# Optimization experiments

Measured on AMD Instinct MI355X. Metric: run time of the kernel, lower is better.

The kernel has to match this reference:

```python
import jax, jax.numpy as jnp
import numpy as np

SEQ, BATCH, N_IN, N_HID, N_OUT = 2048, 64, 256, 512, 128


def setup_inputs() -> dict:
    key = jax.random.key(0)
    ks = jax.random.split(key, 7)
    s_ih = 1.0 / np.sqrt(N_IN)
    s_hh = 1.0 / np.sqrt(N_HID)
    return {
        "x": jax.random.normal(ks[0], (SEQ, BATCH, N_IN), dtype=jnp.float32),
        # PyTorch Linear stores weight as (out_features, in_features)
        "W_ih": jax.random.uniform(ks[1], (N_HID, N_IN), jnp.float32, -s_ih, s_ih),
        "b_ih": jax.random.uniform(ks[2], (N_HID,), jnp.float32, -s_ih, s_ih),
        "W_hh": jax.random.uniform(ks[3], (N_HID, N_HID), jnp.float32, -s_hh, s_hh),
        "b_hh": jax.random.uniform(ks[4], (N_HID,), jnp.float32, -s_hh, s_hh),
        "W_ho": jax.random.uniform(ks[5], (N_OUT, N_HID), jnp.float32, -s_hh, s_hh),
        "b_ho": jax.random.uniform(ks[6], (N_OUT,), jnp.float32, -s_hh, s_hh),
    }


def reference(x, W_ih, b_ih, W_hh, b_hh, W_ho, b_ho):
    # hidden init: torch.zeros(1, n_hidden) broadcasts to (batch, n_hidden)
    h0 = jnp.zeros((x.shape[1], W_hh.shape[0]), dtype=x.dtype)

    def step(h, xt):
        # new_h = tanh(Linear_ih(x_t) + Linear_hh(h))
        h_new = jnp.tanh(xt @ W_ih.T + b_ih + h @ W_hh.T + b_hh)
        return h_new, None

    h_final, _ = jax.lax.scan(step, h0, x)
    return h_final @ W_ho.T + b_ho  # (batch, n_output)
```

## Files before the change

### kernel.cpp

```cpp
#include <hip/hip_runtime.h>
#include <math.h>

#define SEQ   2048
#define BATCH 64
#define NIN   256
#define NHID  512
#define NOUT  128

#define NSL 4
#define JSL 128

#define WIRE_WORDS (2*BATCH*NSL*256)
#define WIRE_BYTES ((size_t)WIRE_WORDS*4)
#define HFIN_BYTES ((size_t)BATCH*NHID*4)
#define XP_BYTES   ((size_t)SEQ*BATCH*NHID*4)

typedef unsigned int u32;
typedef u32 u32x2 __attribute__((ext_vector_type(2)));

__device__ __forceinline__ u32x2 ld8_ic(const u32* p) {
  u32x2 r;
  asm volatile("global_load_dwordx2 %0, %1, off sc0 sc1"
               : "=v"(r) : "v"(p) : "memory");
  return r;
}
__device__ __forceinline__ void st8_ic(u32* p, u32x2 v) {
  asm volatile("global_store_dwordx2 %0, %1, off sc0 sc1"
               :: "v"(p), "v"(v) : "memory");
}
__device__ __forceinline__ void wait_vm0() {
  asm volatile("s_waitcnt vmcnt(0)" ::: "memory");
  __builtin_amdgcn_sched_barrier(0);
}

__global__ __launch_bounds__(256, 1)
void xproj_kernel(const float* __restrict__ x,
                  const float* __restrict__ Wih,
                  const float* __restrict__ bih,
                  const float* __restrict__ bhh,
                  float* __restrict__ xp)
{
  const int bj = blockIdx.x & 7;
  const int bm = blockIdx.x >> 3;
  const int tid = threadIdx.x;
  const int tx = tid & 15, ty = tid >> 4;

  __shared__ __align__(16) float  wT[NIN][68];
  __shared__ __align__(16) float4 xS[64][66];

  for (int it = 0; it < 64; ++it) {
    const int widx = tid + (it << 8);
    const int k = widx >> 6, j = widx & 63;
    wT[k][j] = Wih[(size_t)(bj*64 + j)*NIN + k];
  }
  const int jg = bj*64 + tx*4;
  float4 bv;
  bv.x = bih[jg+0]+bhh[jg+0]; bv.y = bih[jg+1]+bhh[jg+1];
  bv.z = bih[jg+2]+bhh[jg+2]; bv.w = bih[jg+3]+bhh[jg+3];
  __syncthreads();

  for (int mt = 0; mt < 8; ++mt) {
    const size_t r0 = (size_t)bm*512 + mt*64;
    for (int it = 0; it < 16; ++it) {
      const int f = tid + (it << 8);
      const int m = f >> 6, kq = f & 63;
      xS[m][kq] = *(const float4*)&x[(r0 + m)*NIN + (kq << 2)];
    }
    __syncthreads();

    float acc[4][4];
    #pragma unroll
    for (int q = 0; q < 4; ++q)
      #pragma unroll
      for (int jj = 0; jj < 4; ++jj) acc[q][jj] = 0.f;

    for (int kq = 0; kq < 64; ++kq) {
      const float4 xv0 = xS[ty*4+0][kq];
      const float4 xv1 = xS[ty*4+1][kq];
      const float4 xv2 = xS[ty*4+2][kq];
      const float4 xv3 = xS[ty*4+3][kq];
      #pragma unroll
      for (int i = 0; i < 4; ++i) {
        const float4 wv = *(const float4*)&wT[(kq<<2)+i][tx*4];
        const float xi0 = (i==0)?xv0.x:(i==1)?xv0.y:(i==2)?xv0.z:xv0.w;
        const float xi1 = (i==0)?xv1.x:(i==1)?xv1.y:(i==2)?xv1.z:xv1.w;
        const float xi2 = (i==0)?xv2.x:(i==1)?xv2.y:(i==2)?xv2.z:xv2.w;
        const float xi3 = (i==0)?xv3.x:(i==1)?xv3.y:(i==2)?xv3.z:xv3.w;
        acc[0][0]=fmaf(xi0,wv.x,acc[0][0]); acc[0][1]=fmaf(xi0,wv.y,acc[0][1]);
        acc[0][2]=fmaf(xi0,wv.z,acc[0][2]); acc[0][3]=fmaf(xi0,wv.w,acc[0][3]);
        acc[1][0]=fmaf(xi1,wv.x,acc[1][0]); acc[1][1]=fmaf(xi1,wv.y,acc[1][1]);
        acc[1][2]=fmaf(xi1,wv.z,acc[1][2]); acc[1][3]=fmaf(xi1,wv.w,acc[1][3]);
        acc[2][0]=fmaf(xi2,wv.x,acc[2][0]); acc[2][1]=fmaf(xi2,wv.y,acc[2][1]);
        acc[2][2]=fmaf(xi2,wv.z,acc[2][2]); acc[2][3]=fmaf(xi2,wv.w,acc[2][3]);
        acc[3][0]=fmaf(xi3,wv.x,acc[3][0]); acc[3][1]=fmaf(xi3,wv.y,acc[3][1]);
        acc[3][2]=fmaf(xi3,wv.z,acc[3][2]); acc[3][3]=fmaf(xi3,wv.w,acc[3][3]);
      }
    }
    #pragma unroll
    for (int q = 0; q < 4; ++q) {
      float4 o;
      o.x = acc[q][0]+bv.x; o.y = acc[q][1]+bv.y;
      o.z = acc[q][2]+bv.z; o.w = acc[q][3]+bv.w;
      *(float4*)&xp[(r0 + ty*4 + q)*NHID + jg] = o;
    }
    __syncthreads();
  }
}

__global__ __launch_bounds__(512, 1)
void rnn_seq4_kernel(const float* __restrict__ xp,
                     const float* __restrict__ Whh,
                     u32* __restrict__ wire,
                     float* __restrict__ hfin)
{
  const int bid = blockIdx.x;
  const int sj  = bid >> 6;
  const int b   = bid & 63;
  const int tid = threadIdx.x;
  const int jg  = tid >> 4;
  const int kl  = tid & 15;
  const int w   = tid >> 6, lane = tid & 63;

  __shared__ __align__(16) float hS[2][16][36];
  for (int i = tid; i < 16*36; i += 512) (&hS[0][0][0])[i] = 0.f;

  const int j0 = sj*JSL + jg*4;
  const int k0 = kl*32;
  float4 w0[8], w1[8], w2[8], w3[8];
  #pragma unroll
  for (int i = 0; i < 8; ++i) {
    w0[i] = *(const float4*)&Whh[(size_t)(j0+0)*NHID + k0 + 4*i];
    w1[i] = *(const float4*)&Whh[(size_t)(j0+1)*NHID + k0 + 4*i];
    w2[i] = *(const float4*)&Whh[(size_t)(j0+2)*NHID + k0 + 4*i];
    w3[i] = *(const float4*)&Whh[(size_t)(j0+3)*NHID + k0 + 4*i];
  }

  const int jl = jg*4 + (kl & 3);
  const float* xpc = xp + (size_t)b*NHID + sj*JSL + jl;
  float xpC = xpc[0];

  const int sp = (sj + 1 + (w >> 1)) & 3;
  const int sm = ((w & 1) << 6) + lane;
  const int srow = sp*4 + (sm >> 5), scol = sm & 31;
  const int orow = sj*4 + (jl >> 5), ocol = jl & 31;

  __syncthreads();

  int par = 0;
  float hnew = 0.f;
  for (int t = 0; t < SEQ; ++t) {
    float xpN = 0.f;
    if (t + 1 < SEQ) xpN = xpc[(size_t)(t+1)*(BATCH*NHID)];

    float a0=0.f, a1=0.f, a2=0.f, a3=0.f;
    #pragma unroll
    for (int i = 0; i < 8; ++i) {
      const float4 hv = *(const float4*)&hS[par][kl][4*i];
      a0=fmaf(w0[i].x,hv.x,a0); a0=fmaf(w0[i].y,hv.y,a0);
      a0=fmaf(w0[i].z,hv.z,a0); a0=fmaf(w0[i].w,hv.w,a0);
      a1=fmaf(w1[i].x,hv.x,a1); a1=fmaf(w1[i].y,hv.y,a1);
      a1=fmaf(w1[i].z,hv.z,a1); a1=fmaf(w1[i].w,hv.w,a1);
      a2=fmaf(w2[i].x,hv.x,a2); a2=fmaf(w2[i].y,hv.y,a2);
      a2=fmaf(w2[i].z,hv.z,a2); a2=fmaf(w2[i].w,hv.w,a2);
      a3=fmaf(w3[i].x,hv.x,a3); a3=fmaf(w3[i].y,hv.y,a3);
      a3=fmaf(w3[i].z,hv.z,a3); a3=fmaf(w3[i].w,hv.w,a3);
    }

    {
      const float t0 = __shfl_xor(a0,1,16), t1 = __shfl_xor(a1,1,16);
      const float t2 = __shfl_xor(a2,1,16), t3 = __shfl_xor(a3,1,16);
      float b0, b1;
      if (kl & 1) { b0 = a1 + t1; b1 = a3 + t3; }
      else        { b0 = a0 + t0; b1 = a2 + t2; }
      const float u0 = __shfl_xor(b0,2,16), u1 = __shfl_xor(b1,2,16);
      float s = (kl & 2) ? (b1 + u1) : (b0 + u0);
      s += __shfl_xor(s, 4, 16);
      s += __shfl_xor(s, 8, 16);
      hnew = tanhf(s + xpC);
    }
    const int par2 = par ^ 1;

    if (t + 1 < SEQ) {
      if (kl < 4) {
        hS[par2][orow][ocol] = hnew;
        const u32 bits = __float_as_uint(hnew);
        const u32 tag  = (u32)(t+1) << 16;
        u32x2 pv; pv.x = tag | (bits >> 16); pv.y = tag | (bits & 0xffffu);
        st8_ic(wire + ((((size_t)par2*BATCH + b)*NSL + sj) << 8) + (jl << 1), pv);
      }
      if (w < 6) {
        const u32* src = wire + ((((size_t)par2*BATCH + b)*NSL + sp) << 8) + (sm << 1);
        const u32 tg = (u32)(t+1);
        u32x2 v = ld8_ic(src);
        wait_vm0();
        int guard = 1 << 17;
        while (!__all((v.x >> 16) == tg && (v.y >> 16) == tg)) {
          if (--guard == 0) break;
          v = ld8_ic(src);
          wait_vm0();
        }
        hS[par2][srow][scol] = __uint_as_float((v.x << 16) | (v.y & 0xffffu));
      }
      __syncthreads();
      xpC = xpN;
      par = par2;
    }
  }
  if (kl < 4) hfin[(size_t)b*NHID + sj*JSL + jl] = hnew;
}

__global__ __launch_bounds__(512, 2)
void rnn_seq_fb_kernel(const float* __restrict__ xp,
                       const float* __restrict__ Whh,
                       float* __restrict__ hfin)
{
  const int b = blockIdx.x;
  const int j = threadIdx.x;
  __shared__ __align__(16) float hh[2][NHID];
  hh[0][j] = 0.f;
  const float* wrow = Whh + (size_t)j*NHID;
  const float* xcol = xp + (size_t)b*NHID + j;
  float xpC = xcol[0];
  float hnew = 0.f;
  __syncthreads();
  for (int t = 0; t < SEQ; ++t) {
    const int par = t & 1;
    float xpN = 0.f;
    if (t + 1 < SEQ) xpN = xcol[(size_t)(t+1)*(BATCH*NHID)];
    const float* hA = hh[par];
    float a0=0.f,a1=0.f,a2=0.f,a3=0.f;
    #pragma unroll 8
    for (int kq = 0; kq < 128; ++kq) {
      const float4 wv = *(const float4*)&wrow[kq << 2];
      const float4 hv = *(const float4*)&hA[kq << 2];
      a0 = fmaf(wv.x, hv.x, a0);
      a1 = fmaf(wv.y, hv.y, a1);
      a2 = fmaf(wv.z, hv.z, a2);
      a3 = fmaf(wv.w, hv.w, a3);
    }
    hnew = tanhf((a0+a1)+(a2+a3) + xpC);
    hh[par ^ 1][j] = hnew;
    xpC = xpN;
    __syncthreads();
  }
  hfin[(size_t)b*NHID + j] = hnew;
}

__global__ __launch_bounds__(NOUT, 1)
void rnn_out_kernel(const float* __restrict__ hfin,
                    const float* __restrict__ Who,
                    const float* __restrict__ bho,
                    float* __restrict__ out)
{
  const int b = blockIdx.x;
  const int o = threadIdx.x;
  __shared__ __align__(16) float hB[NHID];
  for (int k = o; k < NHID; k += NOUT) hB[k] = hfin[(size_t)b*NHID + k];
  __syncthreads();
  const float* wr = Who + (size_t)o*NHID;
  float a0=0.f,a1=0.f,a2=0.f,a3=0.f;
  for (int k = 0; k < NHID; k += 4) {
    const float4 wv = *(const float4*)&wr[k];
    a0 = fmaf(wv.x, hB[k  ], a0);
    a1 = fmaf(wv.y, hB[k+1], a1);
    a2 = fmaf(wv.z, hB[k+2], a2);
    a3 = fmaf(wv.w, hB[k+3], a3);
  }
  out[(size_t)b*NOUT + o] = (a0+a1)+(a2+a3) + bho[o];
}

extern "C" void kernel_launch(void* const* d_in, const int* in_sizes, int n_in,
                              void* d_out, int out_size, void* d_ws, size_t ws_size,
                              hipStream_t stream)
{
  const float* x   = (const float*)d_in[0];
  const float* Wih = (const float*)d_in[1];
  const float* bih = (const float*)d_in[2];
  const float* Whh = (const float*)d_in[3];
  const float* bhh = (const float*)d_in[4];
  const float* Who = (const float*)d_in[5];
  const float* bho = (const float*)d_in[6];
  float* out = (float*)d_out;

  const size_t need = WIRE_BYTES + HFIN_BYTES + XP_BYTES;

  if (ws_size >= need) {
    u32*   wire = (u32*)d_ws;
    float* hfin = (float*)((char*)d_ws + WIRE_BYTES);
    float* xp   = (float*)((char*)d_ws + WIRE_BYTES + HFIN_BYTES);

    hipMemsetAsync(wire, 0, WIRE_BYTES, stream);
    xproj_kernel  <<<dim3(2048), dim3(256), 0, stream>>>(x, Wih, bih, bhh, xp);
    rnn_seq4_kernel<<<dim3(NSL*BATCH), dim3(512), 0, stream>>>(xp, Whh, wire, hfin);
    rnn_out_kernel<<<dim3(BATCH), dim3(NOUT), 0, stream>>>(hfin, Who, bho, out);
  } else {
    float* hfin = (float*)d_ws;
    float* xp   = (float*)((char*)d_ws + HFIN_BYTES);
    xproj_kernel<<<dim3(2048), dim3(256), 0, stream>>>(x, Wih, bih, bhh, xp);
    rnn_seq_fb_kernel<<<dim3(BATCH), dim3(512), 0, stream>>>(xp, Whh, hfin);
    rnn_out_kernel<<<dim3(BATCH), dim3(NOUT), 0, stream>>>(hfin, Who, bho, out);
  }
}
```

Baseline: 4.388 ms.

## Use fast tanh, unroll RNN loop by parity, and widen xproj blocks

Replaces tanhf with an exp2/rcp based fast tanh on the serial recurrence critical path. Unrolls the time loop by two so double-buffer pointers and wire addresses are precomputed constants instead of parity-indexed arithmetic. Narrows the first shuffle reductions to width 4. Doubles the xproj block to 512 threads with fewer rows per thread, trading register tiling reuse for more parallelism. Fast tanh loses some accuracy for large or small inputs.

```diff
diff --git a/kernel.cpp b/kernel.cpp
--- a/kernel.cpp
+++ b/kernel.cpp
@@ -33,7 +33,13 @@
   __builtin_amdgcn_sched_barrier(0);
 }
 
-__global__ __launch_bounds__(256, 1)
+__device__ __forceinline__ float fast_tanh(float x) {
+  const float e = __builtin_amdgcn_exp2f(x * 2.8853900817779268f);
+  const float r = __builtin_amdgcn_rcpf(e + 1.0f);
+  return fmaf(-2.0f, r, 1.0f);
+}
+
+__global__ __launch_bounds__(512, 1)
 void xproj_kernel(const float* __restrict__ x,
                   const float* __restrict__ Wih,
                   const float* __restrict__ bih,
@@ -48,8 +54,8 @@
   __shared__ __align__(16) float  wT[NIN][68];
   __shared__ __align__(16) float4 xS[64][66];
 
-  for (int it = 0; it < 64; ++it) {
-    const int widx = tid + (it << 8);
+  for (int it = 0; it < 32; ++it) {
+    const int widx = tid + (it << 9);
     const int k = widx >> 6, j = widx & 63;
     wT[k][j] = Wih[(size_t)(bj*64 + j)*NIN + k];
   }
@@ -61,48 +67,40 @@
 
   for (int mt = 0; mt < 8; ++mt) {
     const size_t r0 = (size_t)bm*512 + mt*64;
-    for (int it = 0; it < 16; ++it) {
-      const int f = tid + (it << 8);
+    for (int it = 0; it < 8; ++it) {
+      const int f = tid + (it << 9);
       const int m = f >> 6, kq = f & 63;
       xS[m][kq] = *(const float4*)&x[(r0 + m)*NIN + (kq << 2)];
     }
     __syncthreads();
 
-    float acc[4][4];
+    float acc[2][4];
     #pragma unroll
-    for (int q = 0; q < 4; ++q)
+    for (int q = 0; q < 2; ++q)
       #pragma unroll
       for (int jj = 0; jj < 4; ++jj) acc[q][jj] = 0.f;
 
     for (int kq = 0; kq < 64; ++kq) {
-      const float4 xv0 = xS[ty*4+0][kq];
-      const float4 xv1 = xS[ty*4+1][kq];
-      const float4 xv2 = xS[ty*4+2][kq];
-      const float4 xv3 = xS[ty*4+3][kq];
+      const float4 xv0 = xS[ty*2+0][kq];
+      const float4 xv1 = xS[ty*2+1][kq];
       #pragma unroll
       for (int i = 0; i < 4; ++i) {
         const float4 wv = *(const float4*)&wT[(kq<<2)+i][tx*4];
         const float xi0 = (i==0)?xv0.x:(i==1)?xv0.y:(i==2)?xv0.z:xv0.w;
         const float xi1 = (i==0)?xv1.x:(i==1)?xv1.y:(i==2)?xv1.z:xv1.w;
-        const float xi2 = (i==0)?xv2.x:(i==1)?xv2.y:(i==2)?xv2.z:xv2.w;
-        const float xi3 = (i==0)?xv3.x:(i==1)?xv3.y:(i==2)?xv3.z:xv3.w;
         acc[0][0]=fmaf(xi0,wv.x,acc[0][0]); acc[0][1]=fmaf(xi0,wv.y,acc[0][1]);
         acc[0][2]=fmaf(xi0,wv.z,acc[0][2]); acc[0][3]=fmaf(xi0,wv.w,acc[0][3]);
         acc[1][0]=fmaf(xi1,wv.x,acc[1][0]); acc[1][1]=fmaf(xi1,wv.y,acc[1][1]);
         acc[1][2]=fmaf(xi1,wv.z,acc[1][2]); acc[1][3]=fmaf(xi1,wv.w,acc[1][3]);
-        acc[2][0]=fmaf(xi2,wv.x,acc[2][0]); acc[2][1]=fmaf(xi2,wv.y,acc[2][1]);
-        acc[2][2]=fmaf(xi2,wv.z,acc[2][2]); acc[2][3]=fmaf(xi2,wv.w,acc[2][3]);
-        acc[3][0]=fmaf(xi3,wv.x,acc[3][0]); acc[3][1]=fmaf(xi3,wv.y,acc[3][1]);
-        acc[3][2]=fmaf(xi3,wv.z,acc[3][2]); acc[3][3]=fmaf(xi3,wv.w,acc[3][3]);
       }
     }
-    #pragma unroll
-    for (int q = 0; q < 4; ++q) {
-      float4 o;
-      o.x = acc[q][0]+bv.x; o.y = acc[q][1]+bv.y;
-      o.z = acc[q][2]+bv.z; o.w = acc[q][3]+bv.w;
-      *(float4*)&xp[(r0 + ty*4 + q)*NHID + jg] = o;
-    }
+    float4 o0, o1;
+    o0.x = acc[0][0]+bv.x; o0.y = acc[0][1]+bv.y;
+    o0.z = acc[0][2]+bv.z; o0.w = acc[0][3]+bv.w;
+    o1.x = acc[1][0]+bv.x; o1.y = acc[1][1]+bv.y;
+    o1.z = acc[1][2]+bv.z; o1.w = acc[1][3]+bv.w;
+    *(float4*)&xp[(r0 + ty*2 + 0)*NHID + jg] = o0;
+    *(float4*)&xp[(r0 + ty*2 + 1)*NHID + jg] = o1;
     __syncthreads();
   }
 }
@@ -136,77 +134,93 @@
   }
 
   const int jl = jg*4 + (kl & 3);
-  const float* xpc = xp + (size_t)b*NHID + sj*JSL + jl;
-  float xpC = xpc[0];
+  const float* xptr = xp + (size_t)b*NHID + sj*JSL + jl;
+  float xpC = *xptr;
+  xptr += BATCH*NHID;
 
   const int sp = (sj + 1 + (w >> 1)) & 3;
   const int sm = ((w & 1) << 6) + lane;
   const int srow = sp*4 + (sm >> 5), scol = sm & 31;
   const int orow = sj*4 + (jl >> 5), ocol = jl & 31;
 
+  const float* dA0 = &hS[0][kl][0];
+  const float* dA1 = &hS[1][kl][0];
+  float* pL0 = &hS[0][orow][ocol];
+  float* pL1 = &hS[1][orow][ocol];
+  float* sd0 = &hS[0][srow][scol];
+  float* sd1 = &hS[1][srow][scol];
+  u32* wo0 = wire + ((((size_t)0*BATCH + b)*NSL + sj) << 8) + (jl << 1);
+  u32* wo1 = wire + ((((size_t)1*BATCH + b)*NSL + sj) << 8) + (jl << 1);
+  const u32* wf0 = wire + ((((size_t)0*BATCH + b)*NSL + sp) << 8) + (sm << 1);
+  const u32* wf1 = wire + ((((size_t)1*BATCH + b)*NSL + sp) << 8) + (sm << 1);
+
   __syncthreads();
 
-  int par = 0;
-  float hnew = 0.f;
-  for (int t = 0; t < SEQ; ++t) {
-    float xpN = 0.f;
-    if (t + 1 < SEQ) xpN = xpc[(size_t)(t+1)*(BATCH*NHID)];
-
-    float a0=0.f, a1=0.f, a2=0.f, a3=0.f;
-    #pragma unroll
-    for (int i = 0; i < 8; ++i) {
-      const float4 hv = *(const float4*)&hS[par][kl][4*i];
-      a0=fmaf(w0[i].x,hv.x,a0); a0=fmaf(w0[i].y,hv.y,a0);
-      a0=fmaf(w0[i].z,hv.z,a0); a0=fmaf(w0[i].w,hv.w,a0);
-      a1=fmaf(w1[i].x,hv.x,a1); a1=fmaf(w1[i].y,hv.y,a1);
-      a1=fmaf(w1[i].z,hv.z,a1); a1=fmaf(w1[i].w,hv.w,a1);
-      a2=fmaf(w2[i].x,hv.x,a2); a2=fmaf(w2[i].y,hv.y,a2);
-      a2=fmaf(w2[i].z,hv.z,a2); a2=fmaf(w2[i].w,hv.w,a2);
-      a3=fmaf(w3[i].x,hv.x,a3); a3=fmaf(w3[i].y,hv.y,a3);
-      a3=fmaf(w3[i].z,hv.z,a3); a3=fmaf(w3[i].w,hv.w,a3);
-    }
-
-    {
-      const float t0 = __shfl_xor(a0,1,16), t1 = __shfl_xor(a1,1,16);
-      const float t2 = __shfl_xor(a2,1,16), t3 = __shfl_xor(a3,1,16);
-      float b0, b1;
-      if (kl & 1) { b0 = a1 + t1; b1 = a3 + t3; }
-      else        { b0 = a0 + t0; b1 = a2 + t2; }
-      const float u0 = __shfl_xor(b0,2,16), u1 = __shfl_xor(b1,2,16);
-      float s = (kl & 2) ? (b1 + u1) : (b0 + u0);
-      s += __shfl_xor(s, 4, 16);
-      s += __shfl_xor(s, 8, 16);
-      hnew = tanhf(s + xpC);
-    }
-    const int par2 = par ^ 1;
-
-    if (t + 1 < SEQ) {
-      if (kl < 4) {
-        hS[par2][orow][ocol] = hnew;
-        const u32 bits = __float_as_uint(hnew);
-        const u32 tag  = (u32)(t+1) << 16;
-        u32x2 pv; pv.x = tag | (bits >> 16); pv.y = tag | (bits & 0xffffu);
-        st8_ic(wire + ((((size_t)par2*BATCH + b)*NSL + sj) << 8) + (jl << 1), pv);
-      }
-      if (w < 6) {
-        const u32* src = wire + ((((size_t)par2*BATCH + b)*NSL + sp) << 8) + (sm << 1);
-        const u32 tg = (u32)(t+1);
-        u32x2 v = ld8_ic(src);
-        wait_vm0();
-        int guard = 1 << 17;
-        while (!__all((v.x >> 16) == tg && (v.y >> 16) == tg)) {
-          if (--guard == 0) break;
-          v = ld8_ic(src);
-          wait_vm0();
-        }
-        hS[par2][srow][scol] = __uint_as_float((v.x << 16) | (v.y & 0xffffu));
-      }
-      __syncthreads();
-      xpC = xpN;
-      par = par2;
-    }
-  }
-  if (kl < 4) hfin[(size_t)b*NHID + sj*JSL + jl] = hnew;
+  float hlast = 0.f;
+
+#define RSTEP(T, DA, PL, WO, WF, SD)                                          \
+  {                                                                           \
+    const bool last_ = (T) == SEQ - 1;                                        \
+    float xpN = 0.f;                                                          \
+    if (!last_) { xpN = *xptr; xptr += BATCH*NHID; }                          \
+    float a0=0.f, a1=0.f, a2=0.f, a3=0.f;                                     \
+    _Pragma("unroll")                                                         \
+    for (int i = 0; i < 8; ++i) {                                             \
+      const float4 hv = *(const float4*)((DA) + 4*i);                         \
+      a0=fmaf(w0[i].x,hv.x,a0); a0=fmaf(w0[i].y,hv.y,a0);                     \
+      a0=fmaf(w0[i].z,hv.z,a0); a0=fmaf(w0[i].w,hv.w,a0);                     \
+      a1=fmaf(w1[i].x,hv.x,a1); a1=fmaf(w1[i].y,hv.y,a1);                     \
+      a1=fmaf(w1[i].z,hv.z,a1); a1=fmaf(w1[i].w,hv.w,a1);                     \
+      a2=fmaf(w2[i].x,hv.x,a2); a2=fmaf(w2[i].y,hv.y,a2);                     \
+      a2=fmaf(w2[i].z,hv.z,a2); a2=fmaf(w2[i].w,hv.w,a2);                     \
+      a3=fmaf(w3[i].x,hv.x,a3); a3=fmaf(w3[i].y,hv.y,a3);                     \
+      a3=fmaf(w3[i].z,hv.z,a3); a3=fmaf(w3[i].w,hv.w,a3);                     \
+    }                                                                         \
+    float s_;                                                                 \
+    {                                                                         \
+      const float t0_ = __shfl_xor(a0,1,4), t1_ = __shfl_xor(a1,1,4);         \
+      const float t2_ = __shfl_xor(a2,1,4), t3_ = __shfl_xor(a3,1,4);         \
+      float b0_, b1_;                                                         \
+      if (kl & 1) { b0_ = a1 + t1_; b1_ = a3 + t3_; }                         \
+      else        { b0_ = a0 + t0_; b1_ = a2 + t2_; }                         \
+      const float u0_ = __shfl_xor(b0_,2,4), u1_ = __shfl_xor(b1_,2,4);       \
+      s_ = (kl & 2) ? (b1_ + u1_) : (b0_ + u0_);                              \
+      s_ += __shfl_xor(s_, 4, 16);                                            \
+      s_ += __shfl_xor(s_, 8, 16);                                            \
+    }                                                                         \
+    const float hn_ = fast_tanh(s_ + xpC);                                    \
+    if (!last_) {                                                             \
+      const u32 tg_ = (u32)(T) + 1u;                                          \
+      if (kl < 4) {                                                           \
+        *(PL) = hn_;                                                          \
+        const u32 bits_ = __float_as_uint(hn_);                               \
+        u32x2 pv_;                                                            \
+        pv_.x = (tg_<<16) | (bits_>>16);                                      \
+        pv_.y = (tg_<<16) | (bits_ & 0xffffu);                                \
+        st8_ic((WO), pv_);                                                    \
+      }                                                                       \
+      if (w < 6) {                                                            \
+        u32x2 v_ = ld8_ic(WF); wait_vm0();                                    \
+        int guard_ = 1 << 17;                                                 \
+        while (!__all((v_.x>>16)==tg_ && (v_.y>>16)==tg_)) {                  \
+          if (--guard_ == 0) break;         \
+          v_ = ld8_ic(WF); wait_vm0();                                        \
+        }                                                                     \
+        *(SD) = __uint_as_float((v_.x<<16) | (v_.y & 0xffffu));               \
+      }                                                                       \
+      __syncthreads();                             \
+      xpC = xpN;                                                              \
+    }                                                                         \
+    hlast = hn_;                                                              \
+  }
+
+  for (int t = 0; t < SEQ; t += 2) {
+    RSTEP(t,     dA0, pL1, wo1, wf1, sd1);
+    RSTEP(t + 1, dA1, pL0, wo0, wf0, sd0);
+  }
+#undef RSTEP
+
+  if (kl < 4) hfin[(size_t)b*NHID + sj*JSL + jl] = hlast;
 }
 
 __global__ __launch_bounds__(512, 2)
@@ -290,13 +304,13 @@
     float* xp   = (float*)((char*)d_ws + WIRE_BYTES + HFIN_BYTES);
 
     hipMemsetAsync(wire, 0, WIRE_BYTES, stream);
-    xproj_kernel  <<<dim3(2048), dim3(256), 0, stream>>>(x, Wih, bih, bhh, xp);
+    xproj_kernel  <<<dim3(2048), dim3(512), 0, stream>>>(x, Wih, bih, bhh, xp);
     rnn_seq4_kernel<<<dim3(NSL*BATCH), dim3(512), 0, stream>>>(xp, Whh, wire, hfin);
     rnn_out_kernel<<<dim3(BATCH), dim3(NOUT), 0, stream>>>(hfin, Who, bho, out);
   } else {
     float* hfin = (float*)d_ws;
     float* xp   = (float*)((char*)d_ws + HFIN_BYTES);
-    xproj_kernel<<<dim3(2048), dim3(256), 0, stream>>>(x, Wih, bih, bhh, xp);
+    xproj_kernel<<<dim3(2048), dim3(512), 0, stream>>>(x, Wih, bih, bhh, xp);
     rnn_seq_fb_kernel<<<dim3(BATCH), dim3(512), 0, stream>>>(xp, Whh, hfin);
     rnn_out_kernel<<<dim3(BATCH), dim3(NOUT), 0, stream>>>(hfin, Who, bho, out);
   }
```

Result: faster. 3.994 ms (-9.0%).
